# Optimization experiments

Hardware: AMD Instinct MI355X
Metric: run time of the kernel (lower is better)

Reference implementation:

```python
import jax, jax.numpy as jnp
import numpy as np

B, S, V, E, HE, HD, MEL_D, MEL_T = 4096, 13, 276, 128, 256, 256, 80, 250

def setup_inputs() -> dict:
    key = jax.random.key(0)
    ks = jax.random.split(key, 20)
    p = lambda k, sh: (jax.random.normal(k, sh, dtype=jnp.float32) * 0.05)
    return {
        'text': jax.random.randint(ks[0], (B, S), 0, V),
        'surprisal': jax.random.normal(ks[1], (B, S), dtype=jnp.float32),
        'emb': p(ks[2], (V, E)),
        'sw': p(ks[3], (E, 1)), 'sb': p(ks[4], (E,)),
        'ew_ih': p(ks[5], (4 * HE, E)), 'ew_hh': p(ks[6], (4 * HE, HE)),
        'eb_ih': p(ks[7], (4 * HE,)), 'eb_hh': p(ks[8], (4 * HE,)),
        'aw': p(ks[9], (1, HD + HE)), 'ab': p(ks[10], (1,)),
        'dw_ih': p(ks[11], (4 * HD, E + HE)), 'dw_hh': p(ks[12], (4 * HD, HD)),
        'db_ih': p(ks[13], (4 * HD,)), 'db_hh': p(ks[14], (4 * HD,)),
        'f1w': p(ks[15], (1024, S * HD)), 'f1b': p(ks[16], (1024,)),
        'f2w': p(ks[17], (MEL_D * MEL_T, 1024)), 'f2b': p(ks[18], (MEL_D * MEL_T,)),
        'init_in': jnp.zeros((E,), dtype=jnp.float32),
    }

def _lstm_cell(x, h, c, w_ih, w_hh, b_ih, b_hh, H):
    # PyTorch gate order: i, f, g, o
    g = x @ w_ih.T + b_ih + h @ w_hh.T + b_hh
    i, f, gg, o = jnp.split(g, 4, axis=-1)
    c2 = jax.nn.sigmoid(f) * c + jax.nn.sigmoid(i) * jnp.tanh(gg)
    h2 = jax.nn.sigmoid(o) * jnp.tanh(c2)
    return h2, c2

def reference(text, surprisal, emb, sw, sb, ew_ih, ew_hh, eb_ih, eb_hh,
              aw, ab, dw_ih, dw_hh, db_ih, db_hh, f1w, f1b, f2w, f2b, init_in):
    # embedding + surprisal projection
    x = emb[text] + (surprisal[..., None] @ sw.T + sb)  # [B,S,E]

    # encoder LSTM over time
    def enc_step(carry, xt):
        h, c = carry
        h2, c2 = _lstm_cell(xt, h, c, ew_ih, ew_hh, eb_ih, eb_hh, HE)
        return (h2, c2), h2
    h0 = jnp.zeros((B, HE), dtype=x.dtype)
    (h_n, c_n), enc_seq = jax.lax.scan(enc_step, (h0, h0), jnp.swapaxes(x, 0, 1))
    enc_out = jnp.swapaxes(enc_seq, 0, 1)  # [B,S,HE]

    # precompute encoder part of attention scores (constant across steps)
    aw_h, aw_e = aw[0, :HD], aw[0, HD:]
    enc_score = enc_out @ aw_e + ab[0]  # [B,S]

    dec_in = jnp.broadcast_to(init_in, (B, E))

    def dec_step(carry, _):
        h, c = carry
        scores = h @ aw_h + 0.0  # [B]
        w = jax.nn.softmax(scores[:, None] + enc_score, axis=1)  # [B,S]
        context = jnp.einsum('bs,bsh->bh', w, enc_out)
        xcat = jnp.concatenate([dec_in, context], axis=-1)
        h2, c2 = _lstm_cell(xcat, h, c, dw_ih, dw_hh, db_ih, db_hh, HD)
        return (h2, c2), h2
    _, dec_seq = jax.lax.scan(dec_step, (h_n, c_n), None, length=S)
    dec_out = jnp.swapaxes(dec_seq, 0, 1).reshape(B, S * HD)  # [B,13*256]

    hfc = jax.nn.relu(dec_out @ f1w.T + f1b)
    out = (hfc @ f2w.T + f2b).reshape(B, MEL_D, MEL_T)
    return out
```

## Files before the change

kernel.cpp:

```cpp
#include <hip/hip_runtime.h>
#include <hip/hip_bf16.h>
#include <stdint.h>
#include <stddef.h>

#define B 4096
#define S 13
#define NG 1024
#define MEL 20000
#define MELP 20480

typedef __attribute__((ext_vector_type(8))) short bf16x8;
typedef __attribute__((ext_vector_type(4))) float f32x4;

__device__ __forceinline__ void g2l16(void* lds, const void* g) {
    __builtin_amdgcn_global_load_lds(
        (const __attribute__((address_space(1))) void*)g,
        (__attribute__((address_space(3))) void*)lds, 16, 0, 0);
}

__device__ __forceinline__ float sigm(float x) { return 1.0f / (1.0f + expf(-x)); }
__device__ __forceinline__ float b2f(unsigned short u) {
    union { float f; unsigned int i; } x; x.i = ((unsigned)u) << 16; return x.f;
}
__device__ __forceinline__ unsigned short f2bu(float f) {
    __hip_bfloat16 h = __float2bfloat16(f);
    return *reinterpret_cast<unsigned short*>(&h);
}
__device__ __forceinline__ bf16x8 cvt8(f32x4 a, f32x4 b) {
    union { bf16x8 v; __hip_bfloat16 e[8]; } u;
    #pragma unroll
    for (int j = 0; j < 4; ++j) { u.e[j] = __float2bfloat16(a[j]); u.e[4 + j] = __float2bfloat16(b[j]); }
    return u.v;
}

__device__ __forceinline__ void swz_decode(int wg, int nwg, int nx, int& bx, int& by) {
    const int cpx = nwg >> 3;
    wg = (wg & 7) * cpx + (wg >> 3);
    const int gsz = nx * 4;
    const int grp = wg / gsz, rem = wg % gsz;
    by = grp * 4 + (rem & 3);
    bx = rem >> 2;
}

#define BAR() do { asm volatile("" ::: "memory"); \
    __builtin_amdgcn_s_barrier(); \
    __builtin_amdgcn_sched_barrier(0); } while (0)

#define P_DECL() \
    __shared__ __hip_bfloat16 As3[4][128 * 32]; \
    __shared__ __hip_bfloat16 Bs3[4][64 * 32]; \
    const int tid  = threadIdx.x; \
    const int lane = tid & 63; \
    const int wv   = tid >> 6; \
    const int l16  = lane & 15; \
    const int sr   = tid >> 2; \
    const int sc   = (((tid & 3) ^ ((tid >> 3) & 3)) << 3); \
    const int sl   = (((lane >> 4) ^ ((l16 >> 1) & 3)) << 3)

#define STG3(buf, k0) do { \
    g2l16(&As3[buf][sr * 32 + (tid & 3) * 8],         Ag + (size_t)sr * K + (k0) + sc); \
    g2l16(&As3[buf][(sr + 64) * 32 + (tid & 3) * 8],  Ag + (size_t)(sr + 64) * K + (k0) + sc); \
    g2l16(&Bs3[buf][sr * 32 + (tid & 3) * 8],         Wg + (size_t)sr * K + (k0) + sc); } while (0)

#define TILE3(cur, stg, k2, DO_STG) do { \
    const __hip_bfloat16* Ab = As3[cur]; \
    const __hip_bfloat16* Bb = Bs3[cur]; \
    bf16x8 af[2], bfr[4]; \
    _Pragma("unroll") for (int m = 0; m < 2; ++m) \
        af[m] = *(const bf16x8*)(Ab + (wv * 32 + m * 16 + l16) * 32 + sl); \
    _Pragma("unroll") for (int n = 0; n < 4; ++n) \
        bfr[n] = *(const bf16x8*)(Bb + (n * 16 + l16) * 32 + sl); \
    if (DO_STG) STG3(stg, k2); \
    __builtin_amdgcn_s_setprio(1); \
    _Pragma("unroll") for (int m = 0; m < 2; ++m) \
        _Pragma("unroll") for (int n = 0; n < 4; ++n) \
            acc[m][n] = __builtin_amdgcn_mfma_f32_16x16x32_bf16(af[m], bfr[n], acc[m][n], 0, 0, 0); \
    __builtin_amdgcn_s_setprio(0); \
} while (0)

#define PIPELINE(K) do { \
    const int nk = (K) >> 5; \
    STG3(0, 0); \
    STG3(1, 32); \
    STG3(2, 64); \
    asm volatile("s_waitcnt vmcnt(6)" ::: "memory"); \
    BAR(); \
    int cur = 0; \
    for (int t = 0; t < nk - 3; ++t) { \
        const int stg = (cur + 3) & 3; \
        TILE3(cur, stg, (t + 3) << 5, true); \
        asm volatile("s_waitcnt vmcnt(6)" ::: "memory"); \
        BAR(); \
        cur = (cur + 1) & 3; \
    } \
    TILE3(cur, 0, 0, false); \
    asm volatile("s_waitcnt vmcnt(3)" ::: "memory"); \
    BAR(); \
    cur = (cur + 1) & 3; \
    TILE3(cur, 0, 0, false); \
    asm volatile("s_waitcnt vmcnt(0)" ::: "memory"); \
    BAR(); \
    cur = (cur + 1) & 3; \
    TILE3(cur, 0, 0, false); \
} while (0)

__global__ __launch_bounds__(256, 2) void gemm3(
    const __hip_bfloat16* __restrict__ A,
    const __hip_bfloat16* __restrict__ W,
    const float* __restrict__ bias,
    float* __restrict__ Cf,
    __hip_bfloat16* __restrict__ Cbf,
    int N, int K, int ldc, int relu, int nx)
{
    P_DECL();
    int bx, by;
    swz_decode(blockIdx.x, gridDim.x, nx, bx, by);
    const int brow = by * 128, bcol = bx * 64;
    const __hip_bfloat16* Ag = A + (size_t)brow * K;
    const __hip_bfloat16* Wg = W + (size_t)bcol * K;
    f32x4 acc[2][4] = {};

    PIPELINE(K);

    const int r4 = (lane >> 4) * 4;
    #pragma unroll
    for (int m = 0; m < 2; ++m) {
        #pragma unroll
        for (int n = 0; n < 4; ++n) {
            const int col = bcol + n * 16 + l16;
            if (col >= N) continue;
            const float bv = bias ? bias[col] : 0.0f;
            #pragma unroll
            for (int r = 0; r < 4; ++r) {
                const int row = brow + wv * 32 + m * 16 + r4 + r;
                float v = acc[m][n][r] + bv;
                if (relu) v = v > 0.0f ? v : 0.0f;
                if (Cf)  Cf[(size_t)row * ldc + col] = v;
                if (Cbf) Cbf[(size_t)row * ldc + col] = __float2bfloat16(v);
            }
        }
    }
}

__global__ __launch_bounds__(256, 2) void gemm_lstm3(
    const __hip_bfloat16* __restrict__ A,
    const __hip_bfloat16* __restrict__ W,
    const float* __restrict__ bias,
    float* __restrict__ c,
    __hip_bfloat16* __restrict__ hb1, int s1,
    __hip_bfloat16* __restrict__ hb2, int s2,
    int K,
    const float* __restrict__ aw,
    float* __restrict__ score)
{
    P_DECL();
    int bx, by;
    swz_decode(blockIdx.x, gridDim.x, 16, bx, by);
    const int brow = by * 128, bcol = bx * 64;
    const __hip_bfloat16* Ag = A + (size_t)brow * K;
    const __hip_bfloat16* Wg = W + (size_t)bcol * K;
    f32x4 acc[2][4] = {};

    PIPELINE(K);

    const int r4 = (lane >> 4) * 4;
    const int unit = bx * 16 + l16;
    const float b0 = bias[bcol + l16];
    const float b1 = bias[bcol + 16 + l16];
    const float b2 = bias[bcol + 32 + l16];
    const float b3 = bias[bcol + 48 + l16];
    const float awe = score ? aw[256 + unit] : 0.0f;
    float ps[2][4];
    #pragma unroll
    for (int m = 0; m < 2; ++m) {
        #pragma unroll
        for (int r = 0; r < 4; ++r) {
            const int row = brow + wv * 32 + m * 16 + r4 + r;
            const float gi = acc[m][0][r] + b0;
            const float gf = acc[m][1][r] + b1;
            const float gg = acc[m][2][r] + b2;
            const float go = acc[m][3][r] + b3;
            const size_t ci = (size_t)row * 256 + unit;
            const float c2 = sigm(gf) * c[ci] + sigm(gi) * tanhf(gg);
            const float h2 = sigm(go) * tanhf(c2);
            c[ci] = c2;
            ps[m][r] = h2 * awe;
            const __hip_bfloat16 hb = __float2bfloat16(h2);
            hb1[(size_t)row * s1 + unit] = hb;
            hb2[(size_t)row * s2 + unit] = hb;
        }
    }
    if (score) {
        #pragma unroll
        for (int m = 0; m < 2; ++m) {
            #pragma unroll
            for (int r = 0; r < 4; ++r) {
                float v = ps[m][r];
                v += __shfl_xor(v, 1);
                v += __shfl_xor(v, 2);
                v += __shfl_xor(v, 4);
                v += __shfl_xor(v, 8);
                if (l16 == 0) {
                    const int row = brow + wv * 32 + m * 16 + r4 + r;
                    atomicAdd(&score[(size_t)row * S], v);
                }
            }
        }
    }
}

__global__ __launch_bounds__(256, 2) void gemm_lstm_dec(
    const __hip_bfloat16* __restrict__ A,
    const __hip_bfloat16* __restrict__ W,
    const float* __restrict__ gctx,
    float* __restrict__ c,
    __hip_bfloat16* __restrict__ hb1,
    __hip_bfloat16* __restrict__ hb2, int s2,
    int K)
{
    P_DECL();
    int bx, by;
    swz_decode(blockIdx.x, gridDim.x, 16, bx, by);
    const int brow = by * 128, bcol = bx * 64;
    const __hip_bfloat16* Ag = A + (size_t)brow * K;
    const __hip_bfloat16* Wg = W + (size_t)bcol * K;
    f32x4 acc[2][4] = {};

    PIPELINE(K);

    const int r4 = (lane >> 4) * 4;
    const int unit = bx * 16 + l16;
    #pragma unroll
    for (int m = 0; m < 2; ++m) {
        #pragma unroll
        for (int r = 0; r < 4; ++r) {
            const int row = brow + wv * 32 + m * 16 + r4 + r;
            const float* g = gctx + (size_t)row * NG + bcol;
            const float gi = acc[m][0][r] + g[l16];
            const float gf = acc[m][1][r] + g[16 + l16];
            const float gg = acc[m][2][r] + g[32 + l16];
            const float go = acc[m][3][r] + g[48 + l16];
            const size_t ci = (size_t)row * 256 + unit;
            const float c2 = sigm(gf) * c[ci] + sigm(gi) * tanhf(gg);
            const float h2 = sigm(go) * tanhf(c2);
            c[ci] = c2;
            const __hip_bfloat16 hb = __float2bfloat16(h2);
            hb1[(size_t)row * 256 + unit] = hb;
            hb2[(size_t)row * s2 + unit] = hb;
        }
    }
}

__global__ __launch_bounds__(512, 2) void gemm256(
    const __hip_bfloat16* __restrict__ A,
    const __hip_bfloat16* __restrict__ W,
    const float* __restrict__ bias,
    float* __restrict__ Cf,
    int N, int K, int ldc, int nx)
{
    __shared__ __hip_bfloat16 As[4][256 * 32];
    __shared__ __hip_bfloat16 Bs[4][256 * 32];
    const int tid  = threadIdx.x;
    const int lane = tid & 63;
    const int wv = tid >> 6, wr = wv >> 2, wc = wv & 3;
    const int l16 = lane & 15;
    int bx, by;
    {
        const int xcd = blockIdx.x & 7;
        const int lid = blockIdx.x >> 3;
        const int st  = lid >> 4;
        const int w   = lid & 15;
        const int gst = xcd * 10 + st;
        const int sbx = gst >> 2;
        const int sby = gst & 3;
        bx = sbx * 4 + (w & 3);
        by = sby * 4 + (w >> 2);
    }
    const int brow = by * 256, bcol = bx * 256;
    const __hip_bfloat16* Ag = A + (size_t)brow * K;
    const __hip_bfloat16* Wg = W + (size_t)bcol * K;
    const int sr = tid >> 2;
    const int sc = (((tid & 3) ^ ((tid >> 3) & 3)) << 3);
    const int sd = tid * 8;
    const int sl = (((lane >> 4) ^ ((l16 >> 1) & 3)) << 3);
    f32x4 acc[8][4] = {};
    const int nk = K >> 5;

    #define STG_A(buf, k0) do { \
        g2l16(&As[buf][sd],        Ag + (size_t)sr * K + (k0) + sc);         \
        g2l16(&As[buf][4096 + sd], Ag + (size_t)(sr + 128) * K + (k0) + sc); } while (0)
    #define STG_B(buf, k0) do { \
        g2l16(&Bs[buf][sd],        Wg + (size_t)sr * K + (k0) + sc);         \
        g2l16(&Bs[buf][4096 + sd], Wg + (size_t)(sr + 128) * K + (k0) + sc); } while (0)

    #define TILE(cur, stg, k2, DO_STG) do {                                    \
        const __hip_bfloat16* Ab = As[cur];                                    \
        const __hip_bfloat16* Bb = Bs[cur];                                    \
        bf16x8 bfr[4], af[4];                                                  \
        _Pragma("unroll") for (int n = 0; n < 4; ++n)                          \
            bfr[n] = *(const bf16x8*)(Bb + (wc * 64 + n * 16 + l16) * 32 + sl);\
        _Pragma("unroll") for (int m = 0; m < 4; ++m)                          \
            af[m] = *(const bf16x8*)(Ab + (wr * 128 + m * 16 + l16) * 32 + sl);\
        if (DO_STG) STG_A(stg, k2);                                            \
        BAR();                                                                 \
        __builtin_amdgcn_s_setprio(1);                                         \
        _Pragma("unroll") for (int m = 0; m < 4; ++m)                          \
            _Pragma("unroll") for (int n = 0; n < 4; ++n)                      \
                acc[m][n] = __builtin_amdgcn_mfma_f32_16x16x32_bf16(           \
                    af[m], bfr[n], acc[m][n], 0, 0, 0);                        \
        __builtin_amdgcn_s_setprio(0);                                         \
        BAR();                                                                 \
        _Pragma("unroll") for (int m = 0; m < 4; ++m)                          \
            af[m] = *(const bf16x8*)(Ab + (wr * 128 + (m + 4) * 16 + l16) * 32 + sl); \
        if (DO_STG) STG_B(stg, k2);                                            \
        BAR();                                                                 \
        __builtin_amdgcn_s_setprio(1);                                         \
        _Pragma("unroll") for (int m = 0; m < 4; ++m)                          \
            _Pragma("unroll") for (int n = 0; n < 4; ++n)                      \
                acc[m + 4][n] = __builtin_amdgcn_mfma_f32_16x16x32_bf16(       \
                    af[m], bfr[n], acc[m + 4][n], 0, 0, 0);                    \
        __builtin_amdgcn_s_setprio(0);                                         \
    } while (0)

    STG_A(0, 0);  STG_B(0, 0);
    STG_A(1, 32); STG_B(1, 32);
    STG_A(2, 64); STG_B(2, 64);
    asm volatile("s_waitcnt vmcnt(8)" ::: "memory");
    BAR();
    int cur = 0;
    for (int t = 0; t < nk - 3; ++t) {
        const int stg = (cur + 3) & 3;
        TILE(cur, stg, (t + 3) << 5, true);
        asm volatile("s_waitcnt vmcnt(8)" ::: "memory");
        BAR();
        cur = (cur + 1) & 3;
    }
    TILE(cur, 0, 0, false);
    asm volatile("s_waitcnt vmcnt(4)" ::: "memory");
    BAR();
    cur = (cur + 1) & 3;
    TILE(cur, 0, 0, false);
    asm volatile("s_waitcnt vmcnt(0)" ::: "memory");
    BAR();
    cur = (cur + 1) & 3;
    TILE(cur, 0, 0, false);

    const int r4 = (lane >> 4) * 4;
    #pragma unroll
    for (int m = 0; m < 8; ++m) {
        #pragma unroll
        for (int n = 0; n < 4; ++n) {
            const int col = bcol + wc * 64 + n * 16 + l16;
            if (col >= N) continue;
            const float bv = bias[col];
            #pragma unroll
            for (int r = 0; r < 4; ++r) {
                const int row = brow + wr * 128 + m * 16 + r4 + r;
                Cf[(size_t)row * ldc + col] = acc[m][n][r] + bv;
            }
        }
    }
}

__device__ __forceinline__ int unperm(int np) {
    const int u = ((np >> 6) << 4) + (np & 15);
    const int g = (np >> 4) & 3;
    return g * 256 + u;
}

#define N_W2   ((long long)MELP * 1024 / 8)
#define N_W1   ((long long)NG * 3328 / 8)
#define N_WE   ((long long)NG * 384 / 8)
#define N_WD   ((long long)NG * 512 / 8)
#define N_EMB  ((long long)B * S * 32)
#define N_INIT ((long long)B * 256)
#define N_F2B  ((long long)MELP)
#define N_BP   ((long long)NG)
#define N_ES   ((long long)B * S)
#define N_PREP (N_W2 + N_W1 + N_WE + N_WD + N_EMB + N_INIT + N_F2B + N_BP + N_ES)

__global__ void prep_all(
    const int* __restrict__ text, const float* __restrict__ surp,
    const float* __restrict__ emb, const float* __restrict__ sw,
    const float* __restrict__ sb,
    const float* __restrict__ ew_ih, const float* __restrict__ ew_hh,
    const float* __restrict__ eb_ih, const float* __restrict__ eb_hh,
    const float* __restrict__ dw_ih, const float* __restrict__ dw_hh,
    const float* __restrict__ db_ih, const float* __restrict__ db_hh,
    const float* __restrict__ f1w, const float* __restrict__ f2w,
    const float* __restrict__ f2b, const float* __restrict__ init_in,
    const float* __restrict__ ab,
    __hip_bfloat16* __restrict__ Wenc,
    __hip_bfloat16* __restrict__ Wdc, __hip_bfloat16* __restrict__ Wdh,
    __hip_bfloat16* __restrict__ W1, __hip_bfloat16* __restrict__ W2,
    float* __restrict__ f2bp, float* __restrict__ be, float* __restrict__ bd,
    __hip_bfloat16* __restrict__ xall, float* __restrict__ c_buf,
    float* __restrict__ enc_score)
{
    long long id = (long long)blockIdx.x * 256 + threadIdx.x;
    if (id < N_W2) {
        const long long i8 = id * 8;
        bf16x8 v;
        if (i8 < (long long)MEL * 1024) {
            v = cvt8(*(const f32x4*)(f2w + i8), *(const f32x4*)(f2w + i8 + 4));
        } else {
            union { bf16x8 w; __hip_bfloat16 e[8]; } u;
            #pragma unroll
            for (int j = 0; j < 8; ++j) u.e[j] = __float2bfloat16(0.0f);
            v = u.w;
        }
        *(bf16x8*)(W2 + i8) = v;
        return;
    }
    id -= N_W2;
    if (id < N_W1) {
        const long long i8 = id * 8;
        *(bf16x8*)(W1 + i8) = cvt8(*(const f32x4*)(f1w + i8), *(const f32x4*)(f1w + i8 + 4));
        return;
    }
    id -= N_W1;
    if (id < N_WE) {
        const int idx = (int)(id * 8);
        const int np = idx / 384, k = idx % 384;
        const int n = unperm(np);
        const float* src = (k < 128) ? (ew_ih + n * 128 + k) : (ew_hh + n * 256 + (k - 128));
        *(bf16x8*)(Wenc + idx) = cvt8(*(const f32x4*)src, *(const f32x4*)(src + 4));
        return;
    }
    id -= N_WE;
    if (id < N_WD) {
        const int idx = (int)(id * 8);
        const int np = idx / 512, k = idx % 512;
        const int n = unperm(np);
        if (k < 256) {
            const float* src = dw_ih + n * 384 + 128 + k;
            *(bf16x8*)(Wdc + np * 256 + k) = cvt8(*(const f32x4*)src, *(const f32x4*)(src + 4));
        } else {
            const float* src = dw_hh + n * 256 + (k - 256);
            *(bf16x8*)(Wdh + np * 256 + (k - 256)) = cvt8(*(const f32x4*)src, *(const f32x4*)(src + 4));
        }
        return;
    }
    id -= N_WD;
    if (id < N_EMB) {
        const int idx = (int)id;
        const int jj = (idx & 31) * 4;
        const int rest = idx >> 5;
        const int b = rest % B;
        const int s = rest / B;
        const float sp = surp[b * S + s];
        const f32x4 e4 = *(const f32x4*)(emb + (size_t)text[b * S + s] * 128 + jj);
        const f32x4 w4 = *(const f32x4*)(sw + jj);
        const f32x4 b4 = *(const f32x4*)(sb + jj);
        __hip_bfloat16* dst = xall + ((size_t)s * B + b) * 384 + jj;
        #pragma unroll
        for (int i = 0; i < 4; ++i) dst[i] = __float2bfloat16(e4[i] + sp * w4[i] + b4[i]);
        return;
    }
    id -= N_EMB;
    if (id < N_INIT) {
        const int idx = (int)id;
        c_buf[idx] = 0.0f;
        const int b = idx >> 8, jj = idx & 255;
        xall[(size_t)b * 384 + 128 + jj] = __float2bfloat16(0.0f);
        return;
    }
    id -= N_INIT;
    if (id < N_F2B) {
        const int idx = (int)id;
        f2bp[idx] = (idx < MEL) ? f2b[idx] : 0.0f;
        return;
    }
    id -= N_F2B;
    if (id < N_BP) {
        const int np = (int)id;
        const int n = unperm(np);
        be[np] = eb_ih[n] + eb_hh[n];
        float s = db_ih[n] + db_hh[n];
        for (int k = 0; k < 128; ++k) s += dw_ih[n * 384 + k] * init_in[k];
        bd[np] = s;
        return;
    }
    id -= N_BP;
    if (id < N_ES) {
        enc_score[id] = ab[0];
        return;
    }
}

__global__ void attn_once(const __hip_bfloat16* __restrict__ enc_out,
                          const float* __restrict__ enc_score,
                          __hip_bfloat16* __restrict__ ctx) {
    int b = (blockIdx.x * 256 + threadIdx.x) >> 6;
    int lane = threadIdx.x & 63;
    if (b >= B) return;
    float sc[S], mx = -1e30f;
    #pragma unroll
    for (int t = 0; t < S; ++t) { sc[t] = enc_score[b * S + t]; mx = fmaxf(mx, sc[t]); }
    float sum = 0.0f;
    #pragma unroll
    for (int t = 0; t < S; ++t) { sc[t] = expf(sc[t] - mx); sum += sc[t]; }
    const float inv = 1.0f / sum;
    float c0 = 0.f, c1 = 0.f, c2 = 0.f, c3 = 0.f;
    #pragma unroll
    for (int t = 0; t < S; ++t) {
        const ushort4 e4 = *(const ushort4*)(enc_out + ((size_t)b * S + t) * 256 + lane * 4);
        const float w = sc[t] * inv;
        c0 += w * b2f(e4.x); c1 += w * b2f(e4.y);
        c2 += w * b2f(e4.z); c3 += w * b2f(e4.w);
    }
    ushort4 o4 = { f2bu(c0), f2bu(c1), f2bu(c2), f2bu(c3) };
    *(ushort4*)(ctx + (size_t)b * 256 + lane * 4) = o4;
}

#define CDIV(a, b) (((a) + (b) - 1) / (b))

extern "C" void kernel_launch(void* const* d_in, const int* in_sizes, int n_in,
                              void* d_out, int out_size, void* d_ws, size_t ws_size,
                              hipStream_t stream) {
    const int*   text    = (const int*)  d_in[0];
    const float* surp    = (const float*)d_in[1];
    const float* emb     = (const float*)d_in[2];
    const float* sw      = (const float*)d_in[3];
    const float* sb      = (const float*)d_in[4];
    const float* ew_ih   = (const float*)d_in[5];
    const float* ew_hh   = (const float*)d_in[6];
    const float* eb_ih   = (const float*)d_in[7];
    const float* eb_hh   = (const float*)d_in[8];
    const float* aw      = (const float*)d_in[9];
    const float* ab      = (const float*)d_in[10];
    const float* dw_ih   = (const float*)d_in[11];
    const float* dw_hh   = (const float*)d_in[12];
    const float* db_ih   = (const float*)d_in[13];
    const float* db_hh   = (const float*)d_in[14];
    const float* f1w     = (const float*)d_in[15];
    const float* f1b     = (const float*)d_in[16];
    const float* f2w     = (const float*)d_in[17];
    const float* f2b     = (const float*)d_in[18];
    const float* init_in = (const float*)d_in[19];
    float* out = (float*)d_out;

    char* p = (char*)d_ws;
    auto alloc = [&](size_t bytes) {
        void* r = (void*)p;
        p += (bytes + 255) & ~(size_t)255;
        return r;
    };
    __hip_bfloat16* Wenc      = (__hip_bfloat16*)alloc((size_t)NG * 384 * 2);
    __hip_bfloat16* Wdc       = (__hip_bfloat16*)alloc((size_t)NG * 256 * 2);
    __hip_bfloat16* Wdh       = (__hip_bfloat16*)alloc((size_t)NG * 256 * 2);
    __hip_bfloat16* W1        = (__hip_bfloat16*)alloc((size_t)NG * 3328 * 2);
    __hip_bfloat16* W2        = (__hip_bfloat16*)alloc((size_t)MELP * 1024 * 2);
    float*          f2bp      = (float*)alloc((size_t)MELP * 4);
    float*          be        = (float*)alloc((size_t)NG * 4);
    float*          bd        = (float*)alloc((size_t)NG * 4);
    __hip_bfloat16* xall      = (__hip_bfloat16*)alloc((size_t)S * B * 384 * 2);
    __hip_bfloat16* enc_out   = (__hip_bfloat16*)alloc((size_t)B * S * 256 * 2);
    float*          enc_score = (float*)alloc((size_t)B * S * 4);
    float*          c_buf     = (float*)alloc((size_t)B * 256 * 4);
    __hip_bfloat16* ctx       = (__hip_bfloat16*)alloc((size_t)B * 256 * 2);
    float*          gctx      = (float*)alloc((size_t)B * NG * 4);
    __hip_bfloat16* hdec      = (__hip_bfloat16*)alloc((size_t)2 * B * 256 * 2);
    __hip_bfloat16* dec_out   = (__hip_bfloat16*)alloc((size_t)B * 3328 * 2);
    __hip_bfloat16* hfc       = (__hip_bfloat16*)alloc((size_t)B * 1024 * 2);
    (void)ws_size; (void)in_sizes; (void)n_in; (void)out_size;

    prep_all<<<(int)CDIV(N_PREP, 256), 256, 0, stream>>>(
        text, surp, emb, sw, sb, ew_ih, ew_hh, eb_ih, eb_hh,
        dw_ih, dw_hh, db_ih, db_hh, f1w, f2w, f2b, init_in, ab,
        Wenc, Wdc, Wdh, W1, W2, f2bp, be, bd, xall, c_buf, enc_score);

    for (int t = 0; t < S; ++t) {
        __hip_bfloat16* hb1; int s1;
        if (t < S - 1) { hb1 = xall + ((size_t)(t + 1) * B * 384) + 128; s1 = 384; }
        else           { hb1 = hdec; s1 = 256; }
        gemm_lstm3<<<512, 256, 0, stream>>>(
            xall + (size_t)t * B * 384, Wenc, be, c_buf,
            hb1, s1, enc_out + (size_t)t * 256, S * 256, 384,
            aw, enc_score + t);
    }

    attn_once<<<CDIV(B * 64, 256), 256, 0, stream>>>(enc_out, enc_score, ctx);
    gemm3<<<(NG / 64) * (B / 128), 256, 0, stream>>>(
        ctx, Wdc, bd, gctx, (__hip_bfloat16*)nullptr, NG, 256, NG, 0, NG / 64);

    for (int t = 0; t < S; ++t) {
        gemm_lstm_dec<<<512, 256, 0, stream>>>(
            hdec + (size_t)(t & 1) * B * 256, Wdh, gctx, c_buf,
            hdec + (size_t)((t + 1) & 1) * B * 256,
            dec_out + (size_t)t * 256, 3328, 256);
    }

    gemm3<<<(NG / 64) * (B / 128), 256, 0, stream>>>(
        dec_out, W1, f1b, (float*)nullptr, hfc, NG, 3328, NG, 1, NG / 64);

    gemm256<<<(MELP / 256) * (B / 256), 512, 0, stream>>>(
        hfc, W2, f2bp, out, MEL, 1024, MEL, MELP / 256);
}
```

Baseline: 609.3 us.

## Replace FC2 256x256 GEMM with 256x128 tile, triple-buffered, higher occupancy

Rewrites the final FC2 GEMM kernel to use 256x128 output tiles with 8 waves each computing 64x64, a 3-stage LDS ring instead of 4, and a single barrier per K step. It also swaps the hand-coded XCD block remap for the shared swz_decode helper and raises the launch bound to 4 blocks per CU. The aim is lower LDS use and more resident blocks to hide latency and reduce barrier overhead. In exchange, each loaded tile is reused across fewer outputs, so more A traffic is needed, and the shallower prefetch ring may expose memory latency.

```diff
diff --git a/kernel.cpp b/kernel.cpp
--- a/kernel.cpp
+++ b/kernel.cpp
@@ -251,103 +251,73 @@
     }
 }
 
-__global__ __launch_bounds__(512, 2) void gemm256(
+__global__ __launch_bounds__(512, 4) void gemm_fc2(
     const __hip_bfloat16* __restrict__ A,
     const __hip_bfloat16* __restrict__ W,
     const float* __restrict__ bias,
     float* __restrict__ Cf,
     int N, int K, int ldc, int nx)
 {
-    __shared__ __hip_bfloat16 As[4][256 * 32];
-    __shared__ __hip_bfloat16 Bs[4][256 * 32];
+    __shared__ __hip_bfloat16 Asf[3][256 * 32];
+    __shared__ __hip_bfloat16 Bsf[3][128 * 32];
     const int tid  = threadIdx.x;
     const int lane = tid & 63;
-    const int wv = tid >> 6, wr = wv >> 2, wc = wv & 3;
-    const int l16 = lane & 15;
+    const int wv   = tid >> 6;
+    const int wr   = wv >> 1, wc = wv & 1;
+    const int l16  = lane & 15;
+    const int sr   = tid >> 2;
+    const int sc   = (((tid & 3) ^ ((tid >> 3) & 3)) << 3);
+    const int sl   = (((lane >> 4) ^ ((l16 >> 1) & 3)) << 3);
     int bx, by;
-    {
-        const int xcd = blockIdx.x & 7;
-        const int lid = blockIdx.x >> 3;
-        const int st  = lid >> 4;
-        const int w   = lid & 15;
-        const int gst = xcd * 10 + st;
-        const int sbx = gst >> 2;
-        const int sby = gst & 3;
-        bx = sbx * 4 + (w & 3);
-        by = sby * 4 + (w >> 2);
-    }
-    const int brow = by * 256, bcol = bx * 256;
+    swz_decode(blockIdx.x, gridDim.x, nx, bx, by);
+    const int brow = by * 256, bcol = bx * 128;
     const __hip_bfloat16* Ag = A + (size_t)brow * K;
     const __hip_bfloat16* Wg = W + (size_t)bcol * K;
-    const int sr = tid >> 2;
-    const int sc = (((tid & 3) ^ ((tid >> 3) & 3)) << 3);
-    const int sd = tid * 8;
-    const int sl = (((lane >> 4) ^ ((l16 >> 1) & 3)) << 3);
-    f32x4 acc[8][4] = {};
+    f32x4 acc[4][4] = {};
     const int nk = K >> 5;
 
-    #define STG_A(buf, k0) do { \
-        g2l16(&As[buf][sd],        Ag + (size_t)sr * K + (k0) + sc);         \
-        g2l16(&As[buf][4096 + sd], Ag + (size_t)(sr + 128) * K + (k0) + sc); } while (0)
-    #define STG_B(buf, k0) do { \
-        g2l16(&Bs[buf][sd],        Wg + (size_t)sr * K + (k0) + sc);         \
-        g2l16(&Bs[buf][4096 + sd], Wg + (size_t)(sr + 128) * K + (k0) + sc); } while (0)
-
-    #define TILE(cur, stg, k2, DO_STG) do {                                    \
-        const __hip_bfloat16* Ab = As[cur];                                    \
-        const __hip_bfloat16* Bb = Bs[cur];                                    \
-        bf16x8 bfr[4], af[4];                                                  \
-        _Pragma("unroll") for (int n = 0; n < 4; ++n)                          \
-            bfr[n] = *(const bf16x8*)(Bb + (wc * 64 + n * 16 + l16) * 32 + sl);\
-        _Pragma("unroll") for (int m = 0; m < 4; ++m)                          \
-            af[m] = *(const bf16x8*)(Ab + (wr * 128 + m * 16 + l16) * 32 + sl);\
-        if (DO_STG) STG_A(stg, k2);                                            \
-        BAR();                                                                 \
-        __builtin_amdgcn_s_setprio(1);                                         \
-        _Pragma("unroll") for (int m = 0; m < 4; ++m)                          \
-            _Pragma("unroll") for (int n = 0; n < 4; ++n)                      \
-                acc[m][n] = __builtin_amdgcn_mfma_f32_16x16x32_bf16(           \
-                    af[m], bfr[n], acc[m][n], 0, 0, 0);                        \
-        __builtin_amdgcn_s_setprio(0);                                         \
-        BAR();                                                                 \
-        _Pragma("unroll") for (int m = 0; m < 4; ++m)                          \
-            af[m] = *(const bf16x8*)(Ab + (wr * 128 + (m + 4) * 16 + l16) * 32 + sl); \
-        if (DO_STG) STG_B(stg, k2);                                            \
-        BAR();                                                                 \
-        __builtin_amdgcn_s_setprio(1);                                         \
-        _Pragma("unroll") for (int m = 0; m < 4; ++m)                          \
-            _Pragma("unroll") for (int n = 0; n < 4; ++n)                      \
-                acc[m + 4][n] = __builtin_amdgcn_mfma_f32_16x16x32_bf16(       \
-                    af[m], bfr[n], acc[m + 4][n], 0, 0, 0);                    \
-        __builtin_amdgcn_s_setprio(0);                                         \
+    #define FSTG(buf, k0) do { \
+        g2l16(&Asf[buf][sr * 32 + (tid & 3) * 8],         Ag + (size_t)sr * K + (k0) + sc); \
+        g2l16(&Asf[buf][(sr + 128) * 32 + (tid & 3) * 8], Ag + (size_t)(sr + 128) * K + (k0) + sc); \
+        g2l16(&Bsf[buf][sr * 32 + (tid & 3) * 8],         Wg + (size_t)sr * K + (k0) + sc); } while (0)
+
+    #define FTILE(cur, stg, k2, DO_STG) do { \
+        const __hip_bfloat16* Ab = Asf[cur]; \
+        const __hip_bfloat16* Bb = Bsf[cur]; \
+        bf16x8 af[4], bfr[4]; \
+        _Pragma("unroll") for (int m = 0; m < 4; ++m) \
+            af[m] = *(const bf16x8*)(Ab + (wr * 64 + m * 16 + l16) * 32 + sl); \
+        _Pragma("unroll") for (int n = 0; n < 4; ++n) \
+            bfr[n] = *(const bf16x8*)(Bb + (wc * 64 + n * 16 + l16) * 32 + sl); \
+        if (DO_STG) FSTG(stg, k2); \
+        __builtin_amdgcn_s_setprio(1); \
+        _Pragma("unroll") for (int m = 0; m < 4; ++m) \
+            _Pragma("unroll") for (int n = 0; n < 4; ++n) \
+                acc[m][n] = __builtin_amdgcn_mfma_f32_16x16x32_bf16(af[m], bfr[n], acc[m][n], 0, 0, 0); \
+        __builtin_amdgcn_s_setprio(0); \
     } while (0)
 
-    STG_A(0, 0);  STG_B(0, 0);
-    STG_A(1, 32); STG_B(1, 32);
-    STG_A(2, 64); STG_B(2, 64);
-    asm volatile("s_waitcnt vmcnt(8)" ::: "memory");
+    FSTG(0, 0);
+    FSTG(1, 32);
+    asm volatile("s_waitcnt vmcnt(3)" ::: "memory");
     BAR();
     int cur = 0;
-    for (int t = 0; t < nk - 3; ++t) {
-        const int stg = (cur + 3) & 3;
-        TILE(cur, stg, (t + 3) << 5, true);
-        asm volatile("s_waitcnt vmcnt(8)" ::: "memory");
+    for (int t = 0; t < nk - 2; ++t) {
+        const int stg = cur >= 1 ? cur - 1 : 2;
+        FTILE(cur, stg, (t + 2) << 5, true);
+        asm volatile("s_waitcnt vmcnt(3)" ::: "memory");
         BAR();
-        cur = (cur + 1) & 3;
-    }
-    TILE(cur, 0, 0, false);
-    asm volatile("s_waitcnt vmcnt(4)" ::: "memory");
-    BAR();
-    cur = (cur + 1) & 3;
-    TILE(cur, 0, 0, false);
+        cur = cur == 2 ? 0 : cur + 1;
+    }
+    FTILE(cur, 0, 0, false);
     asm volatile("s_waitcnt vmcnt(0)" ::: "memory");
     BAR();
-    cur = (cur + 1) & 3;
-    TILE(cur, 0, 0, false);
+    cur = cur == 2 ? 0 : cur + 1;
+    FTILE(cur, 0, 0, false);
 
     const int r4 = (lane >> 4) * 4;
     #pragma unroll
-    for (int m = 0; m < 8; ++m) {
+    for (int m = 0; m < 4; ++m) {
         #pragma unroll
         for (int n = 0; n < 4; ++n) {
             const int col = bcol + wc * 64 + n * 16 + l16;
@@ -355,7 +325,7 @@
             const float bv = bias[col];
             #pragma unroll
             for (int r = 0; r < 4; ++r) {
-                const int row = brow + wr * 128 + m * 16 + r4 + r;
+                const int row = brow + wr * 64 + m * 16 + r4 + r;
                 Cf[(size_t)row * ldc + col] = acc[m][n][r] + bv;
             }
         }
@@ -594,6 +564,6 @@
     gemm3<<<(NG / 64) * (B / 128), 256, 0, stream>>>(
         dec_out, W1, f1b, (float*)nullptr, hfc, NG, 3328, NG, 1, NG / 64);
 
-    gemm256<<<(MELP / 256) * (B / 256), 512, 0, stream>>>(
-        hfc, W2, f2bp, out, MEL, 1024, MEL, MELP / 256);
-}
+    gemm_fc2<<<(MELP / 128) * (B / 256), 512, 0, stream>>>(
+        hfc, W2, f2bp, out, MEL, 1024, MEL, MELP / 128);
+}
```

New measurement: 629.3 us. 1.03x slower.

## Fuse decoder LSTM steps into one persistent kernel with LDS-resident hidden state

Applied to the files above, without the earlier changes.

Replaces the 13 per-step decoder GEMM+LSTM launches with a single persistent kernel. Each block owns 64 batch rows, keeps h in swizzled LDS and c in registers across all steps, and reads Wdh fragments directly from global/L2. The context-gate GEMM output is written gate-interleaved so each unit's four gate values load as one float4. This removes launch overhead and per-step h/c round trips to global memory, but uses only 64 blocks, which risks low occupancy on a large GPU and puts repeated Wdh loads on the critical path.

```diff
diff --git a/kernel.cpp b/kernel.cpp
--- a/kernel.cpp
+++ b/kernel.cpp
@@ -110,7 +110,7 @@
     const float* __restrict__ bias,
     float* __restrict__ Cf,
     __hip_bfloat16* __restrict__ Cbf,
-    int N, int K, int ldc, int relu, int nx)
+    int N, int K, int ldc, int relu, int nx, int remap4)
 {
     P_DECL();
     int bx, by;
@@ -130,13 +130,19 @@
             const int col = bcol + n * 16 + l16;
             if (col >= N) continue;
             const float bv = bias ? bias[col] : 0.0f;
+            int colw = col;
+            if (remap4) {
+                const int u = ((col >> 6) << 4) + (col & 15);
+                const int g = (col >> 4) & 3;
+                colw = u * 4 + g;
+            }
             #pragma unroll
             for (int r = 0; r < 4; ++r) {
                 const int row = brow + wv * 32 + m * 16 + r4 + r;
                 float v = acc[m][n][r] + bv;
                 if (relu) v = v > 0.0f ? v : 0.0f;
-                if (Cf)  Cf[(size_t)row * ldc + col] = v;
-                if (Cbf) Cbf[(size_t)row * ldc + col] = __float2bfloat16(v);
+                if (Cf)  Cf[(size_t)row * ldc + colw] = v;
+                if (Cbf) Cbf[(size_t)row * ldc + colw] = __float2bfloat16(v);
             }
         }
     }
@@ -209,45 +215,91 @@
     }
 }
 
-__global__ __launch_bounds__(256, 2) void gemm_lstm_dec(
-    const __hip_bfloat16* __restrict__ A,
-    const __hip_bfloat16* __restrict__ W,
-    const float* __restrict__ gctx,
-    float* __restrict__ c,
-    __hip_bfloat16* __restrict__ hb1,
-    __hip_bfloat16* __restrict__ hb2, int s2,
-    int K)
+__global__ __launch_bounds__(512, 2) void dec_persist(
+    const __hip_bfloat16* __restrict__ h0,
+    const __hip_bfloat16* __restrict__ Wdh,
+    const float* __restrict__ gctx4,
+    const float* __restrict__ cin,
+    __hip_bfloat16* __restrict__ dec_out)
 {
-    P_DECL();
-    int bx, by;
-    swz_decode(blockIdx.x, gridDim.x, 16, bx, by);
-    const int brow = by * 128, bcol = bx * 64;
-    const __hip_bfloat16* Ag = A + (size_t)brow * K;
-    const __hip_bfloat16* Wg = W + (size_t)bcol * K;
-    f32x4 acc[2][4] = {};
-
-    PIPELINE(K);
-
-    const int r4 = (lane >> 4) * 4;
-    const int unit = bx * 16 + l16;
-    #pragma unroll
-    for (int m = 0; m < 2; ++m) {
-        #pragma unroll
-        for (int r = 0; r < 4; ++r) {
-            const int row = brow + wv * 32 + m * 16 + r4 + r;
-            const float* g = gctx + (size_t)row * NG + bcol;
-            const float gi = acc[m][0][r] + g[l16];
-            const float gf = acc[m][1][r] + g[16 + l16];
-            const float gg = acc[m][2][r] + g[32 + l16];
-            const float go = acc[m][3][r] + g[48 + l16];
-            const size_t ci = (size_t)row * 256 + unit;
-            const float c2 = sigm(gf) * c[ci] + sigm(gi) * tanhf(gg);
-            const float h2 = sigm(go) * tanhf(c2);
-            c[ci] = c2;
-            const __hip_bfloat16 hb = __float2bfloat16(h2);
-            hb1[(size_t)row * 256 + unit] = hb;
-            hb2[(size_t)row * s2 + unit] = hb;
-        }
+    __shared__ char Hs[8 * 64 * 64];
+    const int tid  = threadIdx.x;
+    const int lane = tid & 63;
+    const int w    = tid >> 6;
+    const int l16  = lane & 15;
+    const int lk   = lane >> 4;
+    const int brow = blockIdx.x * 64;
+
+    #pragma unroll
+    for (int i = 0; i < 4; ++i) {
+        const int linear = tid + i * 512;
+        const int row  = (linear >> 2) & 63;
+        const int kt   = linear >> 8;
+        const int slot = linear & 3;
+        const bf16x8 v = *(const bf16x8*)(h0 + (size_t)(brow + row) * 256 + kt * 32 + slot * 8);
+        *(bf16x8*)(Hs + kt * 4096 + row * 64 + ((slot ^ ((row >> 1) & 3)) << 4)) = v;
+    }
+
+    float creg[4][2][4];
+    #pragma unroll
+    for (int m = 0; m < 4; ++m)
+        #pragma unroll
+        for (int h2 = 0; h2 < 2; ++h2)
+            #pragma unroll
+            for (int r = 0; r < 4; ++r)
+                creg[m][h2][r] = cin[(size_t)(brow + m * 16 + lk * 4 + r) * 256 + 32 * w + h2 * 16 + l16];
+
+    const __hip_bfloat16* Wb = Wdh + (size_t)(w * 128) * 256;
+    __syncthreads();
+
+    for (int t = 0; t < S; ++t) {
+        f32x4 acc[4][8] = {};
+        #pragma unroll
+        for (int kt = 0; kt < 8; ++kt) {
+            bf16x8 af[4], bfr[8];
+            #pragma unroll
+            for (int m = 0; m < 4; ++m) {
+                const int row = m * 16 + l16;
+                af[m] = *(const bf16x8*)(Hs + kt * 4096 + row * 64 + ((lk ^ ((row >> 1) & 3)) << 4));
+            }
+            #pragma unroll
+            for (int n = 0; n < 8; ++n)
+                bfr[n] = *(const bf16x8*)(Wb + (size_t)(n * 16 + l16) * 256 + kt * 32 + lk * 8);
+            #pragma unroll
+            for (int m = 0; m < 4; ++m)
+                #pragma unroll
+                for (int n = 0; n < 8; ++n)
+                    acc[m][n] = __builtin_amdgcn_mfma_f32_16x16x32_bf16(af[m], bfr[n], acc[m][n], 0, 0, 0);
+        }
+        __syncthreads();
+        #pragma unroll
+        for (int m = 0; m < 4; ++m) {
+            #pragma unroll
+            for (int r = 0; r < 4; ++r) {
+                const int row = m * 16 + lk * 4 + r;
+                #pragma unroll
+                for (int h2 = 0; h2 < 2; ++h2) {
+                    const int unit = 32 * w + h2 * 16 + l16;
+                    const f32x4 g4 = *(const f32x4*)(gctx4 + (size_t)(brow + row) * 1024 + unit * 4);
+                    const float gi = acc[m][h2 * 4 + 0][r] + g4[0];
+                    const float gf = acc[m][h2 * 4 + 1][r] + g4[1];
+                    const float gg = acc[m][h2 * 4 + 2][r] + g4[2];
+                    const float go = acc[m][h2 * 4 + 3][r] + g4[3];
+                    float& cc = creg[m][h2][r];
+                    const float c2 = sigm(gf) * cc + sigm(gi) * tanhf(gg);
+                    const float hh = sigm(go) * tanhf(c2);
+                    cc = c2;
+                    const unsigned short hb = f2bu(hh);
+                    const int kk = h2 * 16 + l16;
+                    const int slot = kk >> 3;
+                    *(unsigned short*)(Hs + w * 4096 + row * 64 +
+                        ((slot ^ ((row >> 1) & 3)) << 4) + (kk & 7) * 2) = hb;
+                    dec_out[(size_t)(brow + row) * 3328 + t * 256 + unit] =
+                        *reinterpret_cast<const __hip_bfloat16*>(&hb);
+                }
+            }
+        }
+        __syncthreads();
     }
 }
 
@@ -560,7 +612,7 @@
     float*          c_buf     = (float*)alloc((size_t)B * 256 * 4);
     __hip_bfloat16* ctx       = (__hip_bfloat16*)alloc((size_t)B * 256 * 2);
     float*          gctx      = (float*)alloc((size_t)B * NG * 4);
-    __hip_bfloat16* hdec      = (__hip_bfloat16*)alloc((size_t)2 * B * 256 * 2);
+    __hip_bfloat16* hdec      = (__hip_bfloat16*)alloc((size_t)B * 256 * 2);
     __hip_bfloat16* dec_out   = (__hip_bfloat16*)alloc((size_t)B * 3328 * 2);
     __hip_bfloat16* hfc       = (__hip_bfloat16*)alloc((size_t)B * 1024 * 2);
     (void)ws_size; (void)in_sizes; (void)n_in; (void)out_size;
@@ -582,17 +634,12 @@
 
     attn_once<<<CDIV(B * 64, 256), 256, 0, stream>>>(enc_out, enc_score, ctx);
     gemm3<<<(NG / 64) * (B / 128), 256, 0, stream>>>(
-        ctx, Wdc, bd, gctx, (__hip_bfloat16*)nullptr, NG, 256, NG, 0, NG / 64);
-
-    for (int t = 0; t < S; ++t) {
-        gemm_lstm_dec<<<512, 256, 0, stream>>>(
-            hdec + (size_t)(t & 1) * B * 256, Wdh, gctx, c_buf,
-            hdec + (size_t)((t + 1) & 1) * B * 256,
-            dec_out + (size_t)t * 256, 3328, 256);
-    }
+        ctx, Wdc, bd, gctx, (__hip_bfloat16*)nullptr, NG, 256, NG, 0, NG / 64, 1);
+
+    dec_persist<<<64, 512, 0, stream>>>(hdec, Wdh, gctx, c_buf, dec_out);
 
     gemm3<<<(NG / 64) * (B / 128), 256, 0, stream>>>(
-        dec_out, W1, f1b, (float*)nullptr, hfc, NG, 3328, NG, 1, NG / 64);
+        dec_out, W1, f1b, (float*)nullptr, hfc, NG, 3328, NG, 1, NG / 64, 0);
 
     gemm256<<<(MELP / 256) * (B / 256), 512, 0, stream>>>(
         hfc, W2, f2bp, out, MEL, 1024, MEL, MELP / 256);
```

Measured after the change: 1.140 ms. 1.87x slower.
